# Kernel optimization log

Hardware: AMD Instinct MI355X
Metric: run time of the kernel (lower is better)

## Reference

```python
import jax, jax.numpy as jnp
import numpy as np

B, NN, NC, H, V, K = 1024, 16, 16, 64, 100, 8
C = NN + NC
NEG = -1e9


def _ln_all(x, eps=1e-5):
    # torch.layer_norm(x, x.shape): normalize over ALL elements, no affine
    mu = x.mean()
    var = ((x - mu) ** 2).mean()
    return (x - mu) * jax.lax.rsqrt(var + eps)


def _ln_last(x, g, b, eps=1e-5):
    # nn.LayerNorm(H) with affine params
    mu = x.mean(-1, keepdims=True)
    var = ((x - mu) ** 2).mean(-1, keepdims=True)
    return (x - mu) * jax.lax.rsqrt(var + eps) * g + b


def _masked_ln(x, m, eps=1e-5):
    # x: [C,B,H], m: [C,B]; full-tensor layernorm over in-graph nodes only
    cnt = jnp.maximum(m.sum(1) * x.shape[-1], 1.0)
    mu = (x * m[..., None]).sum((1, 2)) / cnt
    d = x - mu[:, None, None]
    var = ((d * d) * m[..., None]).sum((1, 2)) / cnt
    return d * jax.lax.rsqrt(var + eps)[:, None, None]


def _forward(num_data, cat_data, num_w, num_b, cat_emb, fi_w1, fi_b1, fi_g, fi_be,
             fi_w2, fi_b2, gcn1_w, gcn1_b, gcn2_w, gcn2_b, pw1, pb1, pg, pbe, pw2, pb2):
    # numeric columns: Linear(1,H) per column == scalar * w + b
    fe_num = num_data[..., None] * num_w[None] + num_b[None]              # [B,NN,H]
    fe_num = _ln_all(jax.nn.relu(fe_num.reshape(B, NN * H)))
    fe_cat = cat_emb[jnp.arange(NC)[None, :], cat_data]                   # [B,NC,H]
    fe_cat = _ln_all(fe_cat.reshape(B, NC * H))
    feat = jnp.concatenate([fe_num, fe_cat], axis=1)                      # [B,C*H]
    fe3 = feat.reshape(B, C, H)
    # shared feature-importance MLP applied to every column slice (dropout = eval)
    h = _ln_last(jax.nn.relu(fe3 @ fi_w1 + fi_b1), fi_g, fi_be)
    imp = _ln_all((h @ fi_w2 + fi_b2)[..., 0])                            # [B,C]
    fe3 = fe3 * imp[..., None]
    feat = fe3.reshape(B, C * H)
    # top-K column selection per row + masked softmax
    _, idx = jax.lax.top_k(imp, K)                                        # [B,K]
    mask = jnp.zeros((B, C), jnp.float32).at[jnp.arange(B)[:, None], idx].set(1.0)
    p = jax.nn.softmax(jnp.where(mask > 0, imp, NEG), axis=1) * mask      # [B,C]
    # graph c: nodes = rows with column c in their top-K; zero column c,
    # adjacency = P P^T with zero diagonal, softmax over nonzero entries
    mT = mask.T                                                           # [C,B]
    pm = p[None, :, :] * mT[:, :, None] * (1.0 - jnp.eye(C))[:, None, :]  # [C,B,C]
    S = jnp.einsum('cik,cjk->cij', pm, pm)                                # [C,B,B]
    S = S * (1.0 - jnp.eye(B))
    pos = S > 0
    mx = jnp.max(jnp.where(pos, S, -jnp.inf), axis=(1, 2))
    mx = jnp.where(jnp.isfinite(mx), mx, 0.0)
    E = jnp.where(pos, jnp.exp(S - mx[:, None, None]), 0.0)
    Z = E.sum((1, 2))
    w = E / jnp.where(Z > 0, Z, 1.0)[:, None, None]
    # GCNConv normalization: add self-loops (weight 1) for in-graph nodes
    A = w + jnp.eye(B)[None] * mT[:, :, None]
    deg = A.sum(-1)
    dinv = jnp.where(deg > 0, jax.lax.rsqrt(deg), 0.0)
    An = dinv[:, :, None] * A * dinv[:, None, :]                          # [C,B,B]
    x = jnp.einsum('cij,jh->cih', An, feat @ gcn1_w) + gcn1_b
    x = _masked_ln(jax.nn.relu(x), mT)
    x = jnp.einsum('cij,cjh->cih', An, x @ gcn2_w) + gcn2_b
    x = _masked_ln(jax.nn.relu(x), mT)                                    # [C,B,H]
    # reassembly: each row gathers its K graph outputs, ordered by column id
    cols = jnp.sort(idx, axis=1)                                          # [B,K]
    gathered = x[cols, jnp.arange(B)[:, None]]                            # [B,K,H]
    full = jnp.concatenate([gathered, fe3], axis=1).reshape(B, (K + C) * H)
    return _ln_last(jax.nn.relu(full @ pw1 + pb1), pg, pbe) @ pw2 + pb2   # [B,2]


def setup_inputs() -> dict:
    key = jax.random.key(0)
    ks = jax.random.split(key, 12)
    s = 0.05
    f = jnp.float32
    return {
        'num_data': jax.random.normal(ks[0], (B, NN), f),
        'cat_data': jax.random.randint(ks[1], (B, NC), 0, V, jnp.int32),
        'num_w': jax.random.normal(ks[2], (NN, H), f) * s,
        'num_b': jnp.zeros((NN, H), f),
        'cat_emb': jax.random.normal(ks[3], (NC, V, H), f) * s,
        'fi_w1': jax.random.normal(ks[4], (H, H), f) * s,
        'fi_b1': jnp.zeros((H,), f),
        'fi_g': jnp.ones((H,), f),
        'fi_be': jnp.zeros((H,), f),
        'fi_w2': jax.random.normal(ks[5], (H, 1), f) * s,
        'fi_b2': jnp.zeros((1,), f),
        'gcn1_w': jax.random.normal(ks[6], (C * H, H), f) * s,
        'gcn1_b': jnp.zeros((H,), f),
        'gcn2_w': jax.random.normal(ks[7], (H, H), f) * s,
        'gcn2_b': jnp.zeros((H,), f),
        'pw1': jax.random.normal(ks[8], ((K + C) * H, H), f) * s,
        'pb1': jnp.zeros((H,), f),
        'pg': jnp.ones((H,), f),
        'pbe': jnp.zeros((H,), f),
        'pw2': jax.random.normal(ks[9], (H, 2), f) * s,
        'pb2': jnp.zeros((2,), f),
    }


def reference(num_data, cat_data, num_w, num_b, cat_emb, fi_w1, fi_b1, fi_g, fi_be,
              fi_w2, fi_b2, gcn1_w, gcn1_b, gcn2_w, gcn2_b, pw1, pb1, pg, pbe, pw2, pb2):
    return _forward(num_data, cat_data, num_w, num_b, cat_emb, fi_w1, fi_b1, fi_g, fi_be,
                    fi_w2, fi_b2, gcn1_w, gcn1_b, gcn2_w, gcn2_b, pw1, pb1, pg, pbe, pw2, pb2)
```

## Files before the change

kernel.cpp:

```cpp
#include <hip/hip_runtime.h>
#include <hip/hip_bf16.h>

#define BB   1024
#define NNUM 16
#define NCAT 16
#define HH   64
#define VV   100
#define KK   8
#define CC   32
#define CH   2048
#define FULLW 2560

#define OFF_FE3   0u
#define OFF_X1    2097152u
#define OFF_X2    4194304u
#define OFF_G     6291456u
#define OFF_SIMP  6356992u
#define OFF_P     6389760u
#define OFF_ROWE  6422528u
#define OFF_DINV  6455296u
#define OFF_F     6488064u
#define OFF_STATS 6520832u
#define OFF_Z     6520840u
#define OFF_X1S   6520872u
#define OFF_X2S   6520936u
#define OFF_COLS  6521000u
#define OFF_LIST  6529192u
#define OFF_CNT   6561960u
#define OFF_AOFF  6561992u
#define OFF_AN    6562048u

__device__ inline float wsum64(float v){
  #pragma unroll
  for (int o = 32; o; o >>= 1) v += __shfl_xor(v, o);
  return v;
}

__global__ __launch_bounds__(256) void k_init(float* ws){
  int t = threadIdx.x;
  if (t < 8)  ws[OFF_STATS + t] = 0.f;
  if (t < 64) ws[OFF_X1S + t] = 0.f;
  if (t < 64) ws[OFF_X2S + t] = 0.f;
  if (t < 32) ws[OFF_Z + t] = 0.f;
}

__global__ __launch_bounds__(256) void k_fe(const float* __restrict__ nd,
                                            const float* __restrict__ nw,
                                            const float* __restrict__ nb,
                                            const int* __restrict__ cd,
                                            const float* __restrict__ emb,
                                            float* __restrict__ ws){
  float* fe3 = ws + OFF_FE3;
  float lsn = 0.f, lssn = 0.f, lsc = 0.f, lssc = 0.f;
  for (int idx = blockIdx.x*256 + threadIdx.x; idx < 2*BB*NNUM*HH; idx += gridDim.x*256){
    if (idx < BB*NNUM*HH){
      int h = idx & 63, n = (idx >> 6) & 15, b = idx >> 10;
      float v = fmaxf(nd[b*NNUM + n]*nw[n*HH + h] + nb[n*HH + h], 0.f);
      fe3[b*CH + n*HH + h] = v;
      lsn += v; lssn += v*v;
    } else {
      int i2 = idx - BB*NNUM*HH;
      int h = i2 & 63, cc = (i2 >> 6) & 15, b = i2 >> 10;
      int j = cd[b*NCAT + cc];
      float v = emb[((size_t)cc*VV + j)*HH + h];
      fe3[b*CH + (NNUM + cc)*HH + h] = v;
      lsc += v; lssc += v*v;
    }
  }
  __shared__ float sh[16];
  lsn = wsum64(lsn); lssn = wsum64(lssn);
  lsc = wsum64(lsc); lssc = wsum64(lssc);
  int w = threadIdx.x >> 6;
  if ((threadIdx.x & 63) == 0){ sh[w] = lsn; sh[4+w] = lssn; sh[8+w] = lsc; sh[12+w] = lssc; }
  __syncthreads();
  if (threadIdx.x == 0){
    atomicAdd(ws + OFF_STATS + 0, sh[0]+sh[1]+sh[2]+sh[3]);
    atomicAdd(ws + OFF_STATS + 1, sh[4]+sh[5]+sh[6]+sh[7]);
    atomicAdd(ws + OFF_STATS + 2, sh[8]+sh[9]+sh[10]+sh[11]);
    atomicAdd(ws + OFF_STATS + 3, sh[12]+sh[13]+sh[14]+sh[15]);
  }
}

__global__ __launch_bounds__(256) void k_normfe(float* __restrict__ ws){
  const float Ninv = 1.f/1048576.f;
  int idx = blockIdx.x*256 + threadIdx.x;
  float* fe3 = ws + OFF_FE3;
  const float* st = ws + OFF_STATS;
  int r = idx & (CH-1); int c = r >> 6;
  float s, ssq;
  if (c < NNUM){ s = st[0]; ssq = st[1]; } else { s = st[2]; ssq = st[3]; }
  float mu = s*Ninv;
  float var = ssq*Ninv - mu*mu;
  float rs = rsqrtf(var + 1e-5f);
  fe3[idx] = (fe3[idx] - mu)*rs;
}

__global__ __launch_bounds__(256) void k_fi(const float* __restrict__ w1,
                                            const float* __restrict__ b1,
                                            const float* __restrict__ g,
                                            const float* __restrict__ be,
                                            const float* __restrict__ w2,
                                            const float* __restrict__ b2f,
                                            float* __restrict__ ws){
  __shared__ float w1s[64][65];
  __shared__ float xs[4][64];
  int wv = threadIdx.x >> 6, lane = threadIdx.x & 63;
  for (int q = threadIdx.x; q < 4096; q += 256) w1s[q >> 6][q & 63] = w1[q];
  __syncthreads();
  const float* fe3 = ws + OFF_FE3;
  float b1l = b1[lane], gl = g[lane], bel = be[lane], w2l = w2[lane], b2s = b2f[0];
  int gw = blockIdx.x*4 + wv;
  float ls = 0.f, lss = 0.f;
  for (int it = 0; it < 16; ++it){
    int row = gw + 2048*it;
    float x = fe3[(size_t)row*64 + lane];
    xs[wv][lane] = x;
    float t0 = 0.f, t1 = 0.f, t2 = 0.f, t3 = 0.f;
    #pragma unroll
    for (int k = 0; k < 64; k += 4){
      float4 xq = *(const float4*)&xs[wv][k];
      t0 += xq.x*w1s[k][lane];
      t1 += xq.y*w1s[k+1][lane];
      t2 += xq.z*w1s[k+2][lane];
      t3 += xq.w*w1s[k+3][lane];
    }
    float t = (t0+t1) + (t2+t3) + b1l;
    t = fmaxf(t, 0.f);
    float mu = wsum64(t)*(1.f/64.f);
    float d = t - mu;
    float var = wsum64(d*d)*(1.f/64.f);
    float rs = rsqrtf(var + 1e-5f);
    float h1 = d*rs*gl + bel;
    float s = wsum64(h1*w2l) + b2s;
    if (lane == 0) ws[OFF_SIMP + row] = s;
    ls += s; lss += s*s;
  }
  __shared__ float sh[8];
  if (lane == 0){ sh[wv] = ls; sh[4+wv] = lss; }
  __syncthreads();
  if (threadIdx.x == 0){
    atomicAdd(ws + OFF_STATS + 4, sh[0]+sh[1]+sh[2]+sh[3]);
    atomicAdd(ws + OFF_STATS + 5, sh[4]+sh[5]+sh[6]+sh[7]);
  }
}

__global__ __launch_bounds__(256) void k_topk(float* __restrict__ ws){
  int b = blockIdx.x;
  __shared__ float imp[CC];
  if (threadIdx.x < CC){
    const float Ninv = 1.f/32768.f;
    float s4 = ws[OFF_STATS+4], s5 = ws[OFF_STATS+5];
    float mu = s4*Ninv, var = s5*Ninv - mu*mu;
    float rs = rsqrtf(var + 1e-5f);
    imp[threadIdx.x] = (ws[OFF_SIMP + b*CC + threadIdx.x] - mu)*rs;
  }
  __syncthreads();
  if (threadIdx.x == 0){
    unsigned taken = 0;
    float m0 = 0.f;
    for (int t = 0; t < KK; t++){
      float best = -1e30f; int bi = 0;
      for (int c = 0; c < CC; c++){
        if (!((taken >> c) & 1u) && imp[c] > best){ best = imp[c]; bi = c; }
      }
      taken |= 1u << bi;
      if (t == 0) m0 = best;
    }
    float sum = 0.f;
    int* cols = (int*)(ws + OFF_COLS);
    int tn = 0;
    for (int c = 0; c < CC; c++){
      if ((taken >> c) & 1u){ cols[b*KK + tn] = c; tn++; sum += expf(imp[c] - m0); }
    }
    float inv = 1.f/sum;
    for (int c = 0; c < CC; c++){
      float pv = ((taken >> c) & 1u) ? expf(imp[c] - m0)*inv : 0.f;
      ws[OFF_P + b*CC + c] = pv;
    }
  }
  __syncthreads();
  float* fe3 = ws + OFF_FE3;
  for (int kq = threadIdx.x; kq < CH; kq += 256){
    fe3[b*CH + kq] *= imp[kq >> 6];
  }
}

__global__ __launch_bounds__(256) void k_lists(float* __restrict__ ws){
  int c = blockIdx.x;
  __shared__ int cnt_s;
  if (threadIdx.x == 0) cnt_s = 0;
  __syncthreads();
  int* list = (int*)(ws + OFF_LIST);
  for (int b = threadIdx.x; b < BB; b += 256){
    if (ws[OFF_P + b*CC + c] > 0.f){
      int slot = atomicAdd(&cnt_s, 1);
      list[c*BB + slot] = b;
    }
  }
  __syncthreads();
  if (threadIdx.x == 0) ((int*)(ws + OFF_CNT))[c] = cnt_s;
}

__global__ void k_offs(float* __restrict__ ws){
  if (threadIdx.x == 0){
    const int* cnt = (const int*)(ws + OFF_CNT);
    int* aoff = (int*)(ws + OFF_AOFF);
    int acc = 0;
    for (int c = 0; c < CC; c++){ aoff[c] = acc; acc += cnt[c]*cnt[c]; }
    aoff[CC] = acc;
  }
}

__global__ __launch_bounds__(256) void k_G(const float* __restrict__ w1g, float* __restrict__ ws){
  __shared__ float frow[4][CH];
  int wv = threadIdx.x >> 6, lane = threadIdx.x & 63;
  int b = blockIdx.x*4 + wv;
  const float* fe3 = ws + OFF_FE3;
  for (int q = 0; q < 32; q++) frow[wv][q*64 + lane] = fe3[b*CH + q*64 + lane];
  __syncthreads();
  float a0 = 0.f, a1 = 0.f, a2 = 0.f, a3 = 0.f;
  #pragma unroll 8
  for (int k = 0; k < CH; k += 4){
    float4 fq = *(const float4*)&frow[wv][k];
    a0 += fq.x*w1g[(k+0)*64 + lane];
    a1 += fq.y*w1g[(k+1)*64 + lane];
    a2 += fq.z*w1g[(k+2)*64 + lane];
    a3 += fq.w*w1g[(k+3)*64 + lane];
  }
  ws[OFF_G + b*64 + lane] = (a0+a1) + (a2+a3);
}

__global__ __launch_bounds__(256) void k_E(float* __restrict__ ws){
  int c = blockIdx.x;
  int n = ((const int*)(ws + OFF_CNT))[c];
  int r0 = blockIdx.y*32;
  if (r0 >= n) return;
  const int* list = (const int*)(ws + OFF_LIST) + c*BB;
  const float* p = ws + OFF_P;
  int base = ((const int*)(ws + OFF_AOFF))[c];
  float* An = ws + OFF_AN;
  __shared__ float pis[32][36];
  __shared__ float pT[32][72];
  int wv = threadIdx.x >> 6, lane = threadIdx.x & 63;
  for (int idx = threadIdx.x; idx < 1024; idx += 256){
    int r = idx >> 5, u = idx & 31;
    int ii = r0 + r;
    float v = 0.f;
    if (ii < n && u != c) v = p[list[ii]*CC + u];
    pis[r][u] = v;
  }
  float re[8] = {0.f,0.f,0.f,0.f,0.f,0.f,0.f,0.f};
  int rowBase = r0 + wv*8;
  for (int jt = 0; jt < n; jt += 64){
    __syncthreads();
    for (int idx = threadIdx.x; idx < 2048; idx += 256){
      int t = idx & 63, u = idx >> 6;
      int jj = jt + t;
      float v = 0.f;
      if (jj < n) v = p[list[jj]*CC + u];
      pT[u + (idx >> 6 >= 32 ? 0 : 0)][t] = v;
    }
    __syncthreads();
    int jj = jt + lane;
    bool jok = (jj < n);
    #pragma unroll
    for (int r = 0; r < 8; r++){
      int row = rowBase + r;
      if (row < n){
        float4 pi0 = *(const float4*)&pis[wv*8 + r][0];
        float4 pi1 = *(const float4*)&pis[wv*8 + r][4];
        float4 pi2 = *(const float4*)&pis[wv*8 + r][8];
        float4 pi3 = *(const float4*)&pis[wv*8 + r][12];
        float4 pi4 = *(const float4*)&pis[wv*8 + r][16];
        float4 pi5 = *(const float4*)&pis[wv*8 + r][20];
        float4 pi6 = *(const float4*)&pis[wv*8 + r][24];
        float4 pi7 = *(const float4*)&pis[wv*8 + r][28];
        float s0 = pi0.x*pT[0][lane]  + pi1.x*pT[4][lane]  + pi2.x*pT[8][lane]  + pi3.x*pT[12][lane]
                 + pi4.x*pT[16][lane] + pi5.x*pT[20][lane] + pi6.x*pT[24][lane] + pi7.x*pT[28][lane];
        float s1 = pi0.y*pT[1][lane]  + pi1.y*pT[5][lane]  + pi2.y*pT[9][lane]  + pi3.y*pT[13][lane]
                 + pi4.y*pT[17][lane] + pi5.y*pT[21][lane] + pi6.y*pT[25][lane] + pi7.y*pT[29][lane];
        float s2 = pi0.z*pT[2][lane]  + pi1.z*pT[6][lane]  + pi2.z*pT[10][lane] + pi3.z*pT[14][lane]
                 + pi4.z*pT[18][lane] + pi5.z*pT[22][lane] + pi6.z*pT[26][lane] + pi7.z*pT[30][lane];
        float s3 = pi0.w*pT[3][lane]  + pi1.w*pT[7][lane]  + pi2.w*pT[11][lane] + pi3.w*pT[15][lane]
                 + pi4.w*pT[19][lane] + pi5.w*pT[23][lane] + pi6.w*pT[27][lane] + pi7.w*pT[31][lane];
        float S = (s0+s1) + (s2+s3);
        float Ev = 0.f;
        if (jok && jj != row && S > 0.f) Ev = __expf(S);
        if (jok) An[(size_t)base + (size_t)row*n + jj] = Ev;
        re[r] += Ev;
      }
    }
  }
  float zpart = 0.f;
  #pragma unroll
  for (int r = 0; r < 8; r++){
    float rsum = wsum64(re[r]);
    int row = rowBase + r;
    if (lane == 0 && row < n){
      ws[OFF_ROWE + c*BB + row] = rsum;
      zpart += rsum;
    }
  }
  __shared__ float sh[4];
  if (lane == 0) sh[wv] = zpart;
  __syncthreads();
  if (threadIdx.x == 0) atomicAdd(ws + OFF_Z + c, sh[0]+sh[1]+sh[2]+sh[3]);
}

__global__ __launch_bounds__(256) void k_scl(float* __restrict__ ws){
  int c = blockIdx.x;
  int n = ((const int*)(ws + OFF_CNT))[c];
  int ii = blockIdx.y*256 + threadIdx.x;
  if (ii >= n) return;
  float z = ws[OFF_Z + c];
  float zp = (z > 0.f) ? z : 1.f;
  float re = ws[OFF_ROWE + c*BB + ii];
  float di = rsqrtf(re/zp + 1.0f);
  ws[OFF_DINV + c*BB + ii] = di;
  ws[OFF_F    + c*BB + ii] = di*rsqrtf(zp);
}

__global__ __launch_bounds__(256) void k_agg(const float* __restrict__ src, int chanStride,
                                             const float* __restrict__ bias,
                                             float* __restrict__ outb,
                                             float* __restrict__ statsb,
                                             float* __restrict__ ws){
  int c = blockIdx.x;
  int n = ((const int*)(ws + OFF_CNT))[c];
  int r0 = blockIdx.y*32;
  if (r0 >= n) return;
  int base = ((const int*)(ws + OFF_AOFF))[c];
  const int* list = (const int*)(ws + OFF_LIST);
  const float* E = ws + OFF_AN;
  const float* fpos = ws + OFF_F + c*BB;
  const float* dpos = ws + OFF_DINV + c*BB;
  __shared__ float sl[64][64];
  __shared__ float an_s[64][36];
  int wv = threadIdx.x >> 6, lane = threadIdx.x & 63;
  int rw = wv*8;
  float acc[8] = {0.f,0.f,0.f,0.f,0.f,0.f,0.f,0.f};
  for (int jb = 0; jb < n; jb += 64){
    __syncthreads();
    for (int idx = threadIdx.x; idx < 4096; idx += 256){
      int row = idx >> 6, col = idx & 63;
      int jj = jb + row;
      float v = 0.f;
      if (jj < n){
        int jg = list[c*BB + jj];
        v = src[((size_t)c*(size_t)chanStride + (size_t)jg)*64 + col];
      }
      sl[row][col] = v;
    }
    for (int idx = threadIdx.x; idx < 2048; idx += 256){
      int t = idx >> 5, r = idx & 31;
      int jj = jb + t, iig = r0 + r;
      float v = 0.f;
      if (jj < n && iig < n){
        if (jj == iig){ float d = dpos[iig]; v = d*d; }
        else v = E[(size_t)base + (size_t)jj*n + iig]*fpos[jj]*fpos[iig];
      }
      an_s[t][r] = v;
    }
    __syncthreads();
    #pragma unroll 4
    for (int t = 0; t < 64; t++){
      float v = sl[t][lane];
      float4 c0 = *(const float4*)&an_s[t][rw];
      float4 c1 = *(const float4*)&an_s[t][rw+4];
      acc[0] += c0.x*v; acc[1] += c0.y*v; acc[2] += c0.z*v; acc[3] += c0.w*v;
      acc[4] += c1.x*v; acc[5] += c1.y*v; acc[6] += c1.z*v; acc[7] += c1.w*v;
    }
  }
  float bl = bias[lane];
  float s = 0.f, ssq = 0.f;
  #pragma unroll
  for (int r = 0; r < 8; r++){
    int iig = r0 + rw + r;
    if (iig < n){
      float a = fmaxf(acc[r] + bl, 0.f);
      outb[((size_t)c*BB + list[c*BB + iig])*64 + lane] = a;
      s += a; ssq += a*a;
    }
  }
  s = wsum64(s); ssq = wsum64(ssq);
  if (lane == 0 && ssq != 0.f){
    atomicAdd(statsb + 2*c,     s);
    atomicAdd(statsb + 2*c + 1, ssq);
  }
}

__global__ __launch_bounds__(256) void k_y(const float* __restrict__ w2g, float* __restrict__ ws){
  __shared__ float w2s[64][65];
  __shared__ float xs[4][64];
  int wv = threadIdx.x >> 6, lane = threadIdx.x & 63;
  for (int q = threadIdx.x; q < 4096; q += 256) w2s[q >> 6][q & 63] = w2g[q];
  __syncthreads();
  int c = blockIdx.x;
  int n = ((const int*)(ws + OFF_CNT))[c];
  const int* list = (const int*)(ws + OFF_LIST);
  float* x1 = ws + OFF_X1;
  float cntf = fmaxf((float)(n*64), 1.f);
  float mu = ws[OFF_X1S + 2*c]/cntf;
  float var = ws[OFF_X1S + 2*c + 1]/cntf - mu*mu;
  float rs = rsqrtf(var + 1e-5f);
  for (int ii = blockIdx.y*4 + wv; ii < n; ii += 64){
    int i = list[c*BB + ii];
    size_t bse = ((size_t)c*BB + i)*64;
    float xn = (x1[bse + lane] - mu)*rs;
    xs[wv][lane] = xn;
    float y0 = 0.f, y1 = 0.f, y2 = 0.f, y3 = 0.f;
    #pragma unroll
    for (int k = 0; k < 64; k += 4){
      float4 xq = *(const float4*)&xs[wv][k];
      y0 += xq.x*w2s[k][lane];
      y1 += xq.y*w2s[k+1][lane];
      y2 += xq.z*w2s[k+2][lane];
      y3 += xq.w*w2s[k+3][lane];
    }
    x1[bse + lane] = (y0+y1) + (y2+y3);
  }
}

__global__ __launch_bounds__(256) void k_final(const float* __restrict__ pw1,
                                               const float* __restrict__ pb1,
                                               const float* __restrict__ pg,
                                               const float* __restrict__ pbe,
                                               const float* __restrict__ pw2,
                                               const float* __restrict__ pb2,
                                               float* __restrict__ ws,
                                               float* __restrict__ out){
  __shared__ float fr[4][FULLW];
  int wv = threadIdx.x >> 6, lane = threadIdx.x & 63;
  int b = blockIdx.x*4 + wv;
  const int* cols = (const int*)(ws + OFF_COLS);
  const int* cnt  = (const int*)(ws + OFF_CNT);
  const float* x2 = ws + OFF_X2;
  const float* fe3 = ws + OFF_FE3;
  #pragma unroll
  for (int t = 0; t < KK; t++){
    int ct = cols[b*KK + t];
    float cf = fmaxf((float)(cnt[ct]*64), 1.f);
    float mu = ws[OFF_X2S + 2*ct]/cf;
    float var = ws[OFF_X2S + 2*ct + 1]/cf - mu*mu;
    float rs = rsqrtf(var + 1e-5f);
    fr[wv][t*64 + lane] = (x2[((size_t)ct*BB + b)*64 + lane] - mu)*rs;
  }
  #pragma unroll
  for (int q = 0; q < 32; q++) fr[wv][512 + q*64 + lane] = fe3[b*CH + q*64 + lane];
  __syncthreads();
  float a0 = 0.f, a1 = 0.f, a2 = 0.f, a3 = 0.f;
  #pragma unroll 8
  for (int k = 0; k < FULLW; k += 4){
    float4 fq = *(const float4*)&fr[wv][k];
    a0 += fq.x*pw1[(k+0)*64 + lane];
    a1 += fq.y*pw1[(k+1)*64 + lane];
    a2 += fq.z*pw1[(k+2)*64 + lane];
    a3 += fq.w*pw1[(k+3)*64 + lane];
  }
  float acc = (a0+a1) + (a2+a3) + pb1[lane];
  acc = fmaxf(acc, 0.f);
  float mu = wsum64(acc)*(1.f/64.f);
  float d = acc - mu;
  float var = wsum64(d*d)*(1.f/64.f);
  float rs = rsqrtf(var + 1e-5f);
  float zn = d*rs*pg[lane] + pbe[lane];
  float s0 = wsum64(zn*pw2[lane*2 + 0]);
  float s1 = wsum64(zn*pw2[lane*2 + 1]);
  if (lane == 0){
    out[b*2 + 0] = s0 + pb2[0];
    out[b*2 + 1] = s1 + pb2[1];
  }
}

extern "C" void kernel_launch(void* const* d_in, const int* in_sizes, int n_in,
                              void* d_out, int out_size, void* d_ws, size_t ws_size,
                              hipStream_t stream){
  (void)in_sizes; (void)n_in; (void)out_size; (void)ws_size;
  const float* num_data = (const float*)d_in[0];
  const int*   cat_data = (const int*)d_in[1];
  const float* num_w   = (const float*)d_in[2];
  const float* num_b   = (const float*)d_in[3];
  const float* cat_emb = (const float*)d_in[4];
  const float* fi_w1   = (const float*)d_in[5];
  const float* fi_b1   = (const float*)d_in[6];
  const float* fi_g    = (const float*)d_in[7];
  const float* fi_be   = (const float*)d_in[8];
  const float* fi_w2   = (const float*)d_in[9];
  const float* fi_b2   = (const float*)d_in[10];
  const float* gcn1_w  = (const float*)d_in[11];
  const float* gcn1_b  = (const float*)d_in[12];
  const float* gcn2_w  = (const float*)d_in[13];
  const float* gcn2_b  = (const float*)d_in[14];
  const float* pw1     = (const float*)d_in[15];
  const float* pb1     = (const float*)d_in[16];
  const float* pg      = (const float*)d_in[17];
  const float* pbe     = (const float*)d_in[18];
  const float* pw2     = (const float*)d_in[19];
  const float* pb2     = (const float*)d_in[20];
  float* ws  = (float*)d_ws;
  float* out = (float*)d_out;

  k_init<<<1, 256, 0, stream>>>(ws);
  k_fe<<<2048, 256, 0, stream>>>(num_data, num_w, num_b, cat_data, cat_emb, ws);
  k_normfe<<<8192, 256, 0, stream>>>(ws);
  k_fi<<<512, 256, 0, stream>>>(fi_w1, fi_b1, fi_g, fi_be, fi_w2, fi_b2, ws);
  k_topk<<<1024, 256, 0, stream>>>(ws);
  k_lists<<<32, 256, 0, stream>>>(ws);
  k_offs<<<1, 64, 0, stream>>>(ws);
  k_G<<<256, 256, 0, stream>>>(gcn1_w, ws);
  k_E<<<dim3(32, 32), 256, 0, stream>>>(ws);
  k_scl<<<dim3(32, 4), 256, 0, stream>>>(ws);
  k_agg<<<dim3(32, 32), 256, 0, stream>>>(ws + OFF_G, 0, gcn1_b, ws + OFF_X1, ws + OFF_X1S, ws);
  k_y<<<dim3(32, 16), 256, 0, stream>>>(gcn2_w, ws);
  k_agg<<<dim3(32, 32), 256, 0, stream>>>(ws + OFF_X1, BB, gcn2_b, ws + OFF_X2, ws + OFF_X2S, ws);
  k_final<<<256, 256, 0, stream>>>(pw1, pb1, pg, pbe, pw2, pb2, ws, out);
}
```

Measured before the change: 604.9 us.

## Rewrite graph aggregation as one wave per output row with contiguous E reads

The aggregation kernel moves from a shared-memory tiled scheme (32 rows per block, 64-neighbour tiles of features and a transposed adjacency) to one wavefront per output row. Each wave walks its adjacency row contiguously, gathers neighbour feature rows straight from global memory and adds the diagonal term separately. The old tile read E with a strided, column-wise pattern, and this change removes that along with the LDS staging and the block barriers. In exchange there is no reuse of neighbour features across rows, so every wave gathers them again and relies on cache. Per-block stats are combined in shared memory before the atomics, and the grid grows to 256 y-blocks.

Result: slower. 633.0 us (+4.6%).

```diff
diff --git a/kernel.cpp b/kernel.cpp
--- a/kernel.cpp
+++ b/kernel.cpp
@@ -258,7 +258,7 @@
       int jj = jt + t;
       float v = 0.f;
       if (jj < n) v = p[list[jj]*CC + u];
-      pT[u + (idx >> 6 >= 32 ? 0 : 0)][t] = v;
+      pT[u][t] = v;
     }
     __syncthreads();
     int jj = jt + lane;
@@ -327,65 +327,50 @@
                                              float* __restrict__ ws){
   int c = blockIdx.x;
   int n = ((const int*)(ws + OFF_CNT))[c];
-  int r0 = blockIdx.y*32;
-  if (r0 >= n) return;
-  int base = ((const int*)(ws + OFF_AOFF))[c];
-  const int* list = (const int*)(ws + OFF_LIST);
-  const float* E = ws + OFF_AN;
-  const float* fpos = ws + OFF_F + c*BB;
-  const float* dpos = ws + OFF_DINV + c*BB;
-  __shared__ float sl[64][64];
-  __shared__ float an_s[64][36];
-  int wv = threadIdx.x >> 6, lane = threadIdx.x & 63;
-  int rw = wv*8;
-  float acc[8] = {0.f,0.f,0.f,0.f,0.f,0.f,0.f,0.f};
-  for (int jb = 0; jb < n; jb += 64){
-    __syncthreads();
-    for (int idx = threadIdx.x; idx < 4096; idx += 256){
-      int row = idx >> 6, col = idx & 63;
-      int jj = jb + row;
-      float v = 0.f;
-      if (jj < n){
-        int jg = list[c*BB + jj];
-        v = src[((size_t)c*(size_t)chanStride + (size_t)jg)*64 + col];
+  int wv = __builtin_amdgcn_readfirstlane(threadIdx.x >> 6);
+  int lane = threadIdx.x & 63;
+  int ii = blockIdx.y*4 + wv;
+  bool active = (ii < n);
+  float s = 0.f, ssq = 0.f;
+  if (active){
+    int base = ((const int*)(ws + OFF_AOFF))[c];
+    const int* lst = (const int*)(ws + OFF_LIST) + c*BB;
+    const float* Erow = ws + OFF_AN + (size_t)base + (size_t)ii*n;
+    const float* f = ws + OFF_F + c*BB;
+    const float* srcc = src + (size_t)c*(size_t)chanStride*64;
+    float acc = 0.f;
+    int j = 0;
+    for (; j + 16 <= n; j += 16){
+      #pragma unroll
+      for (int t = 0; t < 16; t++){
+        float ef = Erow[j+t]*f[j+t];
+        int jg = lst[j+t];
+        acc += ef * srcc[(size_t)jg*64 + lane];
       }
-      sl[row][col] = v;
-    }
-    for (int idx = threadIdx.x; idx < 2048; idx += 256){
-      int t = idx >> 5, r = idx & 31;
-      int jj = jb + t, iig = r0 + r;
-      float v = 0.f;
-      if (jj < n && iig < n){
-        if (jj == iig){ float d = dpos[iig]; v = d*d; }
-        else v = E[(size_t)base + (size_t)jj*n + iig]*fpos[jj]*fpos[iig];
-      }
-      an_s[t][r] = v;
-    }
-    __syncthreads();
-    #pragma unroll 4
-    for (int t = 0; t < 64; t++){
-      float v = sl[t][lane];
-      float4 c0 = *(const float4*)&an_s[t][rw];
-      float4 c1 = *(const float4*)&an_s[t][rw+4];
-      acc[0] += c0.x*v; acc[1] += c0.y*v; acc[2] += c0.z*v; acc[3] += c0.w*v;
-      acc[4] += c1.x*v; acc[5] += c1.y*v; acc[6] += c1.z*v; acc[7] += c1.w*v;
-    }
-  }
-  float bl = bias[lane];
-  float s = 0.f, ssq = 0.f;
-  #pragma unroll
-  for (int r = 0; r < 8; r++){
-    int iig = r0 + rw + r;
-    if (iig < n){
-      float a = fmaxf(acc[r] + bl, 0.f);
-      outb[((size_t)c*BB + list[c*BB + iig])*64 + lane] = a;
-      s += a; ssq += a*a;
-    }
-  }
-  s = wsum64(s); ssq = wsum64(ssq);
-  if (lane == 0 && ssq != 0.f){
-    atomicAdd(statsb + 2*c,     s);
-    atomicAdd(statsb + 2*c + 1, ssq);
+    }
+    for (; j < n; j++){
+      float ef = Erow[j]*f[j];
+      int jg = lst[j];
+      acc += ef * srcc[(size_t)jg*64 + lane];
+    }
+    int i = lst[ii];
+    float di = ws[OFF_DINV + c*BB + ii];
+    float srow = srcc[(size_t)i*64 + lane];
+    float a = f[ii]*acc + di*di*srow + bias[lane];
+    a = fmaxf(a, 0.f);
+    outb[((size_t)c*BB + i)*64 + lane] = a;
+    s = wsum64(a); ssq = wsum64(a*a);
+  }
+  __shared__ float shs[4], shq[4];
+  if (lane == 0){ shs[wv] = active ? s : 0.f; shq[wv] = active ? ssq : 0.f; }
+  __syncthreads();
+  if (threadIdx.x == 0){
+    float ts = shs[0]+shs[1]+shs[2]+shs[3];
+    float tq = shq[0]+shq[1]+shq[2]+shq[3];
+    if (tq != 0.f){
+      atomicAdd(statsb + 2*c,     ts);
+      atomicAdd(statsb + 2*c + 1, tq);
+    }
   }
 }
 
@@ -510,8 +495,8 @@
   k_G<<<256, 256, 0, stream>>>(gcn1_w, ws);
   k_E<<<dim3(32, 32), 256, 0, stream>>>(ws);
   k_scl<<<dim3(32, 4), 256, 0, stream>>>(ws);
-  k_agg<<<dim3(32, 32), 256, 0, stream>>>(ws + OFF_G, 0, gcn1_b, ws + OFF_X1, ws + OFF_X1S, ws);
+  k_agg<<<dim3(32, 256), 256, 0, stream>>>(ws + OFF_G, 0, gcn1_b, ws + OFF_X1, ws + OFF_X1S, ws);
   k_y<<<dim3(32, 16), 256, 0, stream>>>(gcn2_w, ws);
-  k_agg<<<dim3(32, 32), 256, 0, stream>>>(ws + OFF_X1, BB, gcn2_b, ws + OFF_X2, ws + OFF_X2S, ws);
+  k_agg<<<dim3(32, 256), 256, 0, stream>>>(ws + OFF_X1, BB, gcn2_b, ws + OFF_X2, ws + OFF_X2S, ws);
   k_final<<<256, 256, 0, stream>>>(pw1, pb1, pg, pbe, pw2, pb2, ws, out);
 }
```
